# Kernel tuning notes

Measured on AMD Instinct MI355X. Metric: run time of the kernel, lower is better.

## Reference

```python
import jax, jax.numpy as jnp
import numpy as np

OUT_FEATURES = 512
IN_FEATURES = 512


def _unfold_tt(G1, G2):
    # G1: (1, do0, r, di0), G2: (r, do1, 1, di1)
    # einsum 'abcd,cefg->abefdg' then reshape -> (out_features, in_features)
    W = jnp.einsum('abcd,cefg->abefdg', G1, G2)
    return W.reshape(OUT_FEATURES, IN_FEATURES)


def setup_inputs() -> dict:
    key = jax.random.key(0)
    ks = jax.random.split(key, 5)
    std = np.sqrt(2.0 / IN_FEATURES).astype(np.float32)
    x = jax.random.normal(ks[0], (8, 4096, 2 * IN_FEATURES), dtype=jnp.float32)
    G1_R = jax.random.uniform(ks[1], (1, 32, 4, 32), jnp.float32, -std, std)
    G2_R = jax.random.uniform(ks[2], (4, 16, 1, 16), jnp.float32, -std, std)
    G1_I = jax.random.uniform(ks[3], (1, 32, 4, 32), jnp.float32, -std, std)
    G2_I = jax.random.uniform(ks[4], (4, 16, 1, 16), jnp.float32, -std, std)
    bias_real = jnp.zeros((OUT_FEATURES,), jnp.float32)
    bias_imag = jnp.zeros((OUT_FEATURES,), jnp.float32)
    return {"x": x, "G1_R": G1_R, "G2_R": G2_R, "G1_I": G1_I, "G2_I": G2_I,
            "bias_real": bias_real, "bias_imag": bias_imag}


def reference(x, G1_R, G2_R, G1_I, G2_I, bias_real, bias_imag):
    W_real = _unfold_tt(G1_R, G2_R)  # (out, in)
    W_imag = _unfold_tt(G1_I, G2_I)
    x_real, x_imag = jnp.split(x, 2, axis=-1)
    # F.linear(x, W, b) = x @ W.T + b
    out_real = x_real @ W_real.T - x_imag @ W_imag.T + bias_real
    out_imag = x_real @ W_imag.T + x_imag @ W_real.T + bias_imag
    return jnp.concatenate([out_real, out_imag], axis=-1)
```

## Files before the change

kernel.cpp:

```cpp
#include <hip/hip_runtime.h>
#include <hip/hip_bf16.h>
#include <stdint.h>


typedef _Float16 half8 __attribute__((ext_vector_type(8)));
typedef _Float16 half4v __attribute__((ext_vector_type(4)));
typedef float f32x4 __attribute__((ext_vector_type(4)));

typedef __attribute__((address_space(3))) void* lds_ptr_t;
typedef const __attribute__((address_space(1))) void* gbl_ptr_t;

__device__ __forceinline__ void gload_lds16(const void* g, void* s) {
  __builtin_amdgcn_global_load_lds((gbl_ptr_t)g, (lds_ptr_t)s, 16, 0, 0);
}

__global__ void build_bt(const float* __restrict__ G1R, const float* __restrict__ G2R,
                         const float* __restrict__ G1I, const float* __restrict__ G2I,
                         _Float16* __restrict__ BT) {
  int idx = blockIdx.x * 256 + threadIdx.x;
  int n = idx >> 10, k = idx & 1023;
  int o = n & 511, i = k & 511;
  bool imagOut = n >= 512, kHi = k >= 512;
  const float* G1;
  const float* G2;
  float sign = 1.0f;
  if (imagOut == kHi) { G1 = G1R; G2 = G2R; }
  else { G1 = G1I; G2 = G2I; if (!imagOut) sign = -1.0f; }
  int b = o >> 4, e = o & 15, d = i >> 4, g = i & 15;
  float w = 0.0f;
#pragma unroll
  for (int c = 0; c < 4; ++c)
    w += G1[b * 128 + c * 32 + d] * G2[c * 256 + e * 16 + g];
  BT[idx] = (_Float16)(sign * w);
}

__global__ __launch_bounds__(256, 2) void tt_gemm(
    const float* __restrict__ A,
    const _Float16* __restrict__ BT,
    const float* __restrict__ bias_r, const float* __restrict__ bias_i,
    float* __restrict__ C) {
  __shared__ __align__(16) _Float16 Als[128 * 32];
  __shared__ __align__(16) _Float16 Bls[128 * 32];

  const int tid = threadIdx.x;
  const int bid = blockIdx.x;
  const int bid2 = (bid & 7) * 256 + (bid >> 3);
  const int mt = bid2 >> 3, nt = bid2 & 7;
  const int row0 = mt * 128, col0 = nt * 128;

  const int lane = tid & 63, wid = tid >> 6;
  const int wm = wid >> 1, wn = wid & 1;
  const int lr = lane & 15, lq = lane >> 4;

  f32x4 acc[4][4] = {};

  const int brow_base = wid * 32 + (lane >> 2);
  const int bk = (lane & 3) * 8;

  const float* Abase = A + (size_t)row0 * 1024;

  for (int kt = 0; kt < 32; ++kt) {
    const int k0 = kt * 32;
    float4 va[4];
#pragma unroll
    for (int i = 0; i < 4; ++i) {
      int fid = i * 256 + tid;
      int ar = fid >> 3, aq = fid & 7;
      va[i] = *(const float4*)(Abase + (size_t)ar * 1024 + k0 + aq * 4);
    }
    __syncthreads();
#pragma unroll
    for (int i = 0; i < 4; ++i) {
      int fid = i * 256 + tid;
      int ar = fid >> 3, aq = fid & 7;
      half4v h = { (_Float16)va[i].x, (_Float16)va[i].y,
                   (_Float16)va[i].z, (_Float16)va[i].w };
      *(half4v*)&Als[ar * 32 + aq * 4] = h;
    }
#pragma unroll
    for (int j = 0; j < 2; ++j) {
      gload_lds16(BT + (size_t)(col0 + brow_base + j * 16) * 1024 + k0 + bk,
                  (char*)Bls + (wid * 2 + j) * 1024);
    }
    __syncthreads();
    half8 af[4], bf[4];
#pragma unroll
    for (int m = 0; m < 4; ++m)
      af[m] = *(const half8*)&Als[(wm * 64 + m * 16 + lr) * 32 + lq * 8];
#pragma unroll
    for (int n = 0; n < 4; ++n)
      bf[n] = *(const half8*)&Bls[(wn * 64 + n * 16 + lr) * 32 + lq * 8];
#pragma unroll
    for (int m = 0; m < 4; ++m)
#pragma unroll
      for (int n = 0; n < 4; ++n)
        acc[m][n] = __builtin_amdgcn_mfma_f32_16x16x32_f16(af[m], bf[n], acc[m][n], 0, 0, 0);
  }

#pragma unroll
  for (int n = 0; n < 4; ++n) {
    int col = col0 + wn * 64 + n * 16 + lr;
    float bias = (col < 512) ? bias_r[col] : bias_i[col - 512];
#pragma unroll
    for (int m = 0; m < 4; ++m) {
      int r0 = row0 + wm * 64 + m * 16 + lq * 4;
#pragma unroll
      for (int r = 0; r < 4; ++r)
        C[(size_t)(r0 + r) * 1024 + col] = acc[m][n][r] + bias;
    }
  }
}

extern "C" void kernel_launch(void* const* d_in, const int* in_sizes, int n_in,
                              void* d_out, int out_size, void* d_ws, size_t ws_size,
                              hipStream_t stream) {
  const float* x   = (const float*)d_in[0];
  const float* G1R = (const float*)d_in[1];
  const float* G2R = (const float*)d_in[2];
  const float* G1I = (const float*)d_in[3];
  const float* G2I = (const float*)d_in[4];
  const float* br  = (const float*)d_in[5];
  const float* bi  = (const float*)d_in[6];
  float* out = (float*)d_out;
  _Float16* BT = (_Float16*)d_ws;

  build_bt<<<4096, 256, 0, stream>>>(G1R, G2R, G1I, G2I, BT);
  tt_gemm<<<2048, 256, 0, stream>>>(x, BT, br, bi, out);
}
```

Before: 116.9 us.

## Enlarge GEMM tiles to 256x256, double-buffer LDS, pre-swizzle B image, interleave loads with MFMA

The fused complex weight matrix is now written as a tiled, XOR-swizzled LDS image, so each block can copy whole B tiles straight into shared memory without bank conflicts. The GEMM moves to 256x256 tiles with 512 threads, a K step of 64 and double-buffered LDS. Global loads for A and B are split into phases and interleaved with MFMA sub-blocks under s_setprio and explicit barriers. The aim is to hide memory latency and cut sync overhead per FLOP, at the cost of much higher register and LDS use (128 KB LDS per block) and lower occupancy.

```diff
diff --git a/kernel.cpp b/kernel.cpp
--- a/kernel.cpp
+++ b/kernel.cpp
@@ -14,16 +14,23 @@
   __builtin_amdgcn_global_load_lds((gbl_ptr_t)g, (lds_ptr_t)s, 16, 0, 0);
 }
 
+#define BAR() __builtin_amdgcn_s_barrier()
+#define PRIO1() __builtin_amdgcn_s_setprio(1)
+#define PRIO0() __builtin_amdgcn_s_setprio(0)
+
 __global__ void build_bt(const float* __restrict__ G1R, const float* __restrict__ G2R,
                          const float* __restrict__ G1I, const float* __restrict__ G2I,
-                         _Float16* __restrict__ BT) {
+                         _Float16* __restrict__ BTimg) {
   int idx = blockIdx.x * 256 + threadIdx.x;
-  int n = idx >> 10, k = idx & 1023;
+  int kcol = idx & 63;
+  int row  = (idx >> 6) & 255;
+  int kt   = (idx >> 14) & 15;
+  int nt   = idx >> 18;
+  int n = nt * 256 + row;
+  int k = kt * 64 + kcol;
   int o = n & 511, i = k & 511;
   bool imagOut = n >= 512, kHi = k >= 512;
-  const float* G1;
-  const float* G2;
-  float sign = 1.0f;
+  const float* G1; const float* G2; float sign = 1.0f;
   if (imagOut == kHi) { G1 = G1R; G2 = G2R; }
   else { G1 = G1I; G2 = G2I; if (!imagOut) sign = -1.0f; }
   int b = o >> 4, e = o & 15, d = i >> 4, g = i & 15;
@@ -31,82 +38,133 @@
 #pragma unroll
   for (int c = 0; c < 4; ++c)
     w += G1[b * 128 + c * 32 + d] * G2[c * 256 + e * 16 + g];
-  BT[idx] = (_Float16)(sign * w);
+  size_t byteoff = ((size_t)(nt * 16 + kt) << 15) + (size_t)row * 128
+                 + ((kcol * 2) ^ ((row & 7) << 4));
+  *(_Float16*)((char*)BTimg + byteoff) = (_Float16)(sign * w);
 }
 
-__global__ __launch_bounds__(256, 2) void tt_gemm(
+__global__ __launch_bounds__(512, 2) void tt_gemm(
     const float* __restrict__ A,
-    const _Float16* __restrict__ BT,
+    const _Float16* __restrict__ Bimg,
     const float* __restrict__ bias_r, const float* __restrict__ bias_i,
     float* __restrict__ C) {
-  __shared__ __align__(16) _Float16 Als[128 * 32];
-  __shared__ __align__(16) _Float16 Bls[128 * 32];
+  __shared__ __align__(16) _Float16 Als[2][16384];
+  __shared__ __align__(16) _Float16 Bls[2][16384];
 
   const int tid = threadIdx.x;
   const int bid = blockIdx.x;
-  const int bid2 = (bid & 7) * 256 + (bid >> 3);
-  const int mt = bid2 >> 3, nt = bid2 & 7;
-  const int row0 = mt * 128, col0 = nt * 128;
+  const int bid2 = (bid & 7) * 64 + (bid >> 3);
+  const int mt = bid2 >> 2, nt = bid2 & 3;
+  const int row0 = mt * 256, col0 = nt * 256;
 
   const int lane = tid & 63, wid = tid >> 6;
-  const int wm = wid >> 1, wn = wid & 1;
+  const int wm = wid >> 2, wn = wid & 3;
   const int lr = lane & 15, lq = lane >> 4;
 
-  f32x4 acc[4][4] = {};
-
-  const int brow_base = wid * 32 + (lane >> 2);
-  const int bk = (lane & 3) * 8;
-
+  const int arow = tid >> 4;
+  const int acol = (tid & 15) * 4;
   const float* Abase = A + (size_t)row0 * 1024;
 
-  for (int kt = 0; kt < 32; ++kt) {
-    const int k0 = kt * 32;
-    float4 va[4];
+  f32x4 acc[8][4] = {};
+  float4 areg[8];
+  half8 afr[4][2], bfr0[2][2], bfr1[2][2];
+
+  auto aissue = [&](int t, int i0) {
 #pragma unroll
     for (int i = 0; i < 4; ++i) {
-      int fid = i * 256 + tid;
-      int ar = fid >> 3, aq = fid & 7;
-      va[i] = *(const float4*)(Abase + (size_t)ar * 1024 + k0 + aq * 4);
+      int ii = i0 + i;
+      areg[ii] = *(const float4*)(Abase + (size_t)(ii * 32 + arow) * 1024 + t * 64 + acol);
     }
-    __syncthreads();
+  };
+  auto awrite = [&](int cb, int i0) {
 #pragma unroll
     for (int i = 0; i < 4; ++i) {
-      int fid = i * 256 + tid;
-      int ar = fid >> 3, aq = fid & 7;
-      half4v h = { (_Float16)va[i].x, (_Float16)va[i].y,
-                   (_Float16)va[i].z, (_Float16)va[i].w };
-      *(half4v*)&Als[ar * 32 + aq * 4] = h;
+      int ii = i0 + i;
+      int row = ii * 32 + arow;
+      int byte = row * 128 + (((tid & 15) * 8) ^ ((row & 7) << 4));
+      half4v h = { (_Float16)areg[ii].x, (_Float16)areg[ii].y,
+                   (_Float16)areg[ii].z, (_Float16)areg[ii].w };
+      *(half4v*)((char*)&Als[cb][0] + byte) = h;
     }
+  };
+  auto bissue = [&](int t, int cb) {
+    const char* src = (const char*)Bimg + (((size_t)nt * 16 + t) << 15) + wid * 4096 + lane * 16;
+    char* dst = (char*)&Bls[cb][0] + wid * 4096;
 #pragma unroll
-    for (int j = 0; j < 2; ++j) {
-      gload_lds16(BT + (size_t)(col0 + brow_base + j * 16) * 1024 + k0 + bk,
-                  (char*)Bls + (wid * 2 + j) * 1024);
-    }
-    __syncthreads();
-    half8 af[4], bf[4];
+    for (int j = 0; j < 4; ++j)
+      gload_lds16(src + j * 1024, dst + j * 1024);
+  };
+  auto lda = [&](int cb, int mh) {
 #pragma unroll
-    for (int m = 0; m < 4; ++m)
-      af[m] = *(const half8*)&Als[(wm * 64 + m * 16 + lr) * 32 + lq * 8];
+    for (int mf = 0; mf < 4; ++mf)
 #pragma unroll
-    for (int n = 0; n < 4; ++n)
-      bf[n] = *(const half8*)&Bls[(wn * 64 + n * 16 + lr) * 32 + lq * 8];
+      for (int kk = 0; kk < 2; ++kk) {
+        int row = wm * 128 + mh * 64 + mf * 16 + lr;
+        int byte = row * 128 + ((kk * 64 + lq * 16) ^ ((row & 7) << 4));
+        afr[mf][kk] = *(const half8*)((const char*)&Als[cb][0] + byte);
+      }
+  };
+  auto ldb = [&](int cb, int nh, half8 (&bf)[2][2]) {
 #pragma unroll
-    for (int m = 0; m < 4; ++m)
+    for (int j = 0; j < 2; ++j)
 #pragma unroll
-      for (int n = 0; n < 4; ++n)
-        acc[m][n] = __builtin_amdgcn_mfma_f32_16x16x32_f16(af[m], bf[n], acc[m][n], 0, 0, 0);
+      for (int kk = 0; kk < 2; ++kk) {
+        int row = wn * 64 + (nh * 2 + j) * 16 + lr;
+        int byte = row * 128 + ((kk * 64 + lq * 16) ^ ((row & 7) << 4));
+        bf[j][kk] = *(const half8*)((const char*)&Bls[cb][0] + byte);
+      }
+  };
+  auto mma = [&](int mh, int nh, half8 (&bf)[2][2]) {
+#pragma unroll
+    for (int mf = 0; mf < 4; ++mf)
+#pragma unroll
+      for (int j = 0; j < 2; ++j)
+#pragma unroll
+        for (int kk = 0; kk < 2; ++kk)
+          acc[mh * 4 + mf][nh * 2 + j] = __builtin_amdgcn_mfma_f32_16x16x32_f16(
+              afr[mf][kk], bf[j][kk], acc[mh * 4 + mf][nh * 2 + j], 0, 0, 0);
+  };
+
+  aissue(0, 0); aissue(0, 4);
+  bissue(0, 0);
+  awrite(0, 0); awrite(0, 4);
+  asm volatile("s_waitcnt vmcnt(0) lgkmcnt(0)" ::: "memory");
+  BAR();
+
+  for (int t = 0; t < 16; ++t) {
+    const int c = t & 1, c2 = c ^ 1;
+    const bool pf = (t < 15);
+    lda(c, 0); ldb(c, 0, bfr0);
+    if (pf) aissue(t + 1, 0);
+    BAR();
+    PRIO1(); mma(0, 0, bfr0); PRIO0();
+    BAR();
+    ldb(c, 1, bfr1);
+    if (pf) aissue(t + 1, 4);
+    BAR();
+    PRIO1(); mma(0, 1, bfr1); PRIO0();
+    BAR();
+    lda(c, 1);
+    if (pf) { bissue(t + 1, c2); awrite(c2, 0); }
+    BAR();
+    PRIO1(); mma(1, 1, bfr1); PRIO0();
+    BAR();
+    if (pf) awrite(c2, 4);
+    PRIO1(); mma(1, 0, bfr0); PRIO0();
+    asm volatile("s_waitcnt vmcnt(0) lgkmcnt(0)" ::: "memory");
+    BAR();
   }
 
 #pragma unroll
-  for (int n = 0; n < 4; ++n) {
-    int col = col0 + wn * 64 + n * 16 + lr;
+  for (int fn = 0; fn < 4; ++fn) {
+    int col = col0 + wn * 64 + fn * 16 + lr;
     float bias = (col < 512) ? bias_r[col] : bias_i[col - 512];
 #pragma unroll
-    for (int m = 0; m < 4; ++m) {
-      int r0 = row0 + wm * 64 + m * 16 + lq * 4;
+    for (int fm = 0; fm < 8; ++fm) {
+      int r0 = row0 + wm * 128 + fm * 16 + lq * 4;
 #pragma unroll
       for (int r = 0; r < 4; ++r)
-        C[(size_t)(r0 + r) * 1024 + col] = acc[m][n][r] + bias;
+        C[(size_t)(r0 + r) * 1024 + col] = acc[fm][fn][r] + bias;
     }
   }
 }
@@ -122,8 +180,8 @@
   const float* br  = (const float*)d_in[5];
   const float* bi  = (const float*)d_in[6];
   float* out = (float*)d_out;
-  _Float16* BT = (_Float16*)d_ws;
+  _Float16* BTimg = (_Float16*)d_ws;
 
-  build_bt<<<4096, 256, 0, stream>>>(G1R, G2R, G1I, G2I, BT);
-  tt_gemm<<<2048, 256, 0, stream>>>(x, BT, br, bi, out);
+  build_bt<<<4096, 256, 0, stream>>>(G1R, G2R, G1I, G2I, BTimg);
+  tt_gemm<<<512, 512, 0, stream>>>(x, BTimg, br, bi, out);
 }
```

Result: slower. 136.9 us (+17.1%).

## Pre-tile fp16 A/B images and use double-buffered 256x256 GEMM pipeline

Applied to the files above, without the earlier changes.

Adds a pre-pass that converts x to fp16 and writes it, along with the unfolded weight, into swizzled 64-wide K tiles, so the GEMM can stage both operands straight into LDS with global_load_lds. The GEMM moves to 256x256 tiles with 512 threads, double-buffered LDS, interleaved MFMA quarters, barriers and s_setprio to overlap loads with compute. The extra conversion pass writes and rereads a 64 MB intermediate, and if the workspace is too small the old path is used instead.

```diff
diff --git a/kernel.cpp b/kernel.cpp
--- a/kernel.cpp
+++ b/kernel.cpp
@@ -14,16 +14,161 @@
   __builtin_amdgcn_global_load_lds((gbl_ptr_t)g, (lds_ptr_t)s, 16, 0, 0);
 }
 
+#define BARF() asm volatile("s_barrier" ::: "memory")
+#define VMCNT0() asm volatile("s_waitcnt vmcnt(0)" ::: "memory")
+#define PRIO1() __builtin_amdgcn_s_setprio(1)
+#define PRIO0() __builtin_amdgcn_s_setprio(0)
+
+
 __global__ void build_bt(const float* __restrict__ G1R, const float* __restrict__ G2R,
                          const float* __restrict__ G1I, const float* __restrict__ G2I,
-                         _Float16* __restrict__ BT) {
+                         _Float16* __restrict__ BTimg) {
+  int idx = blockIdx.x * 256 + threadIdx.x;
+  int kcol = idx & 63;
+  int row  = (idx >> 6) & 255;
+  int kt   = (idx >> 14) & 15;
+  int nt   = idx >> 18;
+  int n = nt * 256 + row;
+  int k = kt * 64 + kcol;
+  int o = n & 511, i = k & 511;
+  bool imagOut = n >= 512, kHi = k >= 512;
+  const float* G1; const float* G2; float sign = 1.0f;
+  if (imagOut == kHi) { G1 = G1R; G2 = G2R; }
+  else { G1 = G1I; G2 = G2I; if (!imagOut) sign = -1.0f; }
+  int b = o >> 4, e = o & 15, d = i >> 4, g = i & 15;
+  float w = 0.0f;
+#pragma unroll
+  for (int c = 0; c < 4; ++c)
+    w += G1[b * 128 + c * 32 + d] * G2[c * 256 + e * 16 + g];
+  size_t byteoff = ((size_t)(nt * 16 + kt) << 15) + (size_t)row * 128
+                 + ((kcol * 2) ^ ((row & 7) << 4));
+  *(_Float16*)((char*)BTimg + byteoff) = (_Float16)(sign * w);
+}
+
+__global__ __launch_bounds__(256) void build_at(const float* __restrict__ A,
+                                                _Float16* __restrict__ Aimg) {
+  const int tid = threadIdx.x;
+  const int kt = blockIdx.x & 15, mt = blockIdx.x >> 4;
+  const float* src = A + (size_t)mt * 256 * 1024 + kt * 64;
+  char* dst = (char*)Aimg + ((size_t)(mt * 16 + kt) << 15);
+  const int cg = tid & 15;
+  const int rb = tid >> 4;
+#pragma unroll
+  for (int r = 0; r < 16; ++r) {
+    int row = rb + r * 16;
+    float4 v = *(const float4*)(src + (size_t)row * 1024 + cg * 4);
+    half4v h = { (_Float16)v.x, (_Float16)v.y, (_Float16)v.z, (_Float16)v.w };
+    *(half4v*)(dst + row * 128 + ((cg * 8) ^ ((row & 7) << 4))) = h;
+  }
+}
+
+__global__ __launch_bounds__(512, 2) void tt_gemm(
+    const _Float16* __restrict__ Aimg, const _Float16* __restrict__ Bimg,
+    const float* __restrict__ bias_r, const float* __restrict__ bias_i,
+    float* __restrict__ C) {
+  __shared__ __align__(16) _Float16 Als[2][16384];
+  __shared__ __align__(16) _Float16 Bls[2][16384];
+
+  const int tid = threadIdx.x;
+  const int bid = blockIdx.x;
+  const int bid2 = (bid & 7) * 64 + (bid >> 3);
+  const int mt = bid2 >> 2, nt = bid2 & 3;
+
+  const int lane = tid & 63, wid = tid >> 6;
+  const int wm = wid >> 2, wn = wid & 3;
+  const int lr = lane & 15, lq = lane >> 4;
+
+  f32x4 acc[8][4] = {};
+  half8 afr0[4][2], afr1[4][2], bfr0[2][2], bfr1[2][2];
+
+  const char* Abase = (const char*)Aimg + ((size_t)mt << 19);
+  const char* Bbase = (const char*)Bimg + ((size_t)nt << 19);
+  const int soff = wid * 1024 + lane * 16;
+  const int doff = wid * 1024;
+
+  auto stage = [&](const char* base, int t, _Float16* ldsbuf) {
+    const char* s = base + ((size_t)t << 15) + soff;
+    char* d = (char*)ldsbuf + doff;
+#pragma unroll
+    for (int j = 0; j < 4; ++j)
+      gload_lds16(s + j * 8192, d + j * 8192);
+  };
+  auto lda = [&](const _Float16* buf, int mh, half8 (&af)[4][2]) {
+#pragma unroll
+    for (int mf = 0; mf < 4; ++mf)
+#pragma unroll
+      for (int kk = 0; kk < 2; ++kk) {
+        int row = wm * 128 + mh * 64 + mf * 16 + lr;
+        int byte = row * 128 + ((kk * 64 + lq * 16) ^ ((row & 7) << 4));
+        af[mf][kk] = *(const half8*)((const char*)buf + byte);
+      }
+  };
+  auto ldb = [&](const _Float16* buf, int nh, half8 (&bf)[2][2]) {
+#pragma unroll
+    for (int j = 0; j < 2; ++j)
+#pragma unroll
+      for (int kk = 0; kk < 2; ++kk) {
+        int row = wn * 64 + (nh * 2 + j) * 16 + lr;
+        int byte = row * 128 + ((kk * 64 + lq * 16) ^ ((row & 7) << 4));
+        bf[j][kk] = *(const half8*)((const char*)buf + byte);
+      }
+  };
+  auto mmaq = [&](half8 (&af)[4][2], half8 (&bf)[2][2], int mb, int nb) {
+#pragma unroll
+    for (int mf = 0; mf < 4; ++mf)
+#pragma unroll
+      for (int j = 0; j < 2; ++j)
+#pragma unroll
+        for (int kk = 0; kk < 2; ++kk)
+          acc[mb + mf][nb + j] = __builtin_amdgcn_mfma_f32_16x16x32_f16(
+              af[mf][kk], bf[j][kk], acc[mb + mf][nb + j], 0, 0, 0);
+  };
+
+  stage(Abase, 0, Als[0]);
+  stage(Bbase, 0, Bls[0]);
+  VMCNT0();
+  BARF();
+
+  for (int t = 0; t < 16; ++t) {
+    const int c = t & 1;
+    _Float16* Ac = Als[c];  _Float16* Bc = Bls[c];
+    _Float16* An = Als[c ^ 1]; _Float16* Bn = Bls[c ^ 1];
+    const bool pf = (t < 15);
+    lda(Ac, 0, afr0); ldb(Bc, 0, bfr0);
+    if (pf) stage(Abase, t + 1, An);
+    BARF(); PRIO1(); mmaq(afr0, bfr0, 0, 0); PRIO0(); BARF();
+    ldb(Bc, 1, bfr1);
+    if (pf) stage(Bbase, t + 1, Bn);
+    BARF(); PRIO1(); mmaq(afr0, bfr1, 0, 2); PRIO0(); BARF();
+    lda(Ac, 1, afr1);
+    BARF(); PRIO1(); mmaq(afr1, bfr1, 4, 2); PRIO0(); BARF();
+    VMCNT0();
+    BARF(); PRIO1(); mmaq(afr1, bfr0, 4, 0); PRIO0(); BARF();
+  }
+
+  const int row0 = mt * 256, col0 = nt * 256;
+#pragma unroll
+  for (int fn = 0; fn < 4; ++fn) {
+    int col = col0 + wn * 64 + fn * 16 + lr;
+    float bias = (col < 512) ? bias_r[col] : bias_i[col - 512];
+#pragma unroll
+    for (int fm = 0; fm < 8; ++fm) {
+      int r0 = row0 + wm * 128 + (fm >> 2) * 64 + (fm & 3) * 16 + lq * 4;
+#pragma unroll
+      for (int r = 0; r < 4; ++r)
+        C[(size_t)(r0 + r) * 1024 + col] = acc[fm][fn][r] + bias;
+    }
+  }
+}
+
+__global__ void build_bt_flat(const float* __restrict__ G1R, const float* __restrict__ G2R,
+                              const float* __restrict__ G1I, const float* __restrict__ G2I,
+                              _Float16* __restrict__ BT) {
   int idx = blockIdx.x * 256 + threadIdx.x;
   int n = idx >> 10, k = idx & 1023;
   int o = n & 511, i = k & 511;
   bool imagOut = n >= 512, kHi = k >= 512;
-  const float* G1;
-  const float* G2;
-  float sign = 1.0f;
+  const float* G1; const float* G2; float sign = 1.0f;
   if (imagOut == kHi) { G1 = G1R; G2 = G2R; }
   else { G1 = G1I; G2 = G2I; if (!imagOut) sign = -1.0f; }
   int b = o >> 4, e = o & 15, d = i >> 4, g = i & 15;
@@ -34,31 +179,24 @@
   BT[idx] = (_Float16)(sign * w);
 }
 
-__global__ __launch_bounds__(256, 2) void tt_gemm(
-    const float* __restrict__ A,
-    const _Float16* __restrict__ BT,
+__global__ __launch_bounds__(256, 2) void tt_gemm_fb(
+    const float* __restrict__ A, const _Float16* __restrict__ BT,
     const float* __restrict__ bias_r, const float* __restrict__ bias_i,
     float* __restrict__ C) {
   __shared__ __align__(16) _Float16 Als[128 * 32];
   __shared__ __align__(16) _Float16 Bls[128 * 32];
-
   const int tid = threadIdx.x;
   const int bid = blockIdx.x;
   const int bid2 = (bid & 7) * 256 + (bid >> 3);
   const int mt = bid2 >> 3, nt = bid2 & 7;
   const int row0 = mt * 128, col0 = nt * 128;
-
   const int lane = tid & 63, wid = tid >> 6;
   const int wm = wid >> 1, wn = wid & 1;
   const int lr = lane & 15, lq = lane >> 4;
-
   f32x4 acc[4][4] = {};
-
   const int brow_base = wid * 32 + (lane >> 2);
   const int bk = (lane & 3) * 8;
-
   const float* Abase = A + (size_t)row0 * 1024;
-
   for (int kt = 0; kt < 32; ++kt) {
     const int k0 = kt * 32;
     float4 va[4];
@@ -78,10 +216,9 @@
       *(half4v*)&Als[ar * 32 + aq * 4] = h;
     }
 #pragma unroll
-    for (int j = 0; j < 2; ++j) {
+    for (int j = 0; j < 2; ++j)
       gload_lds16(BT + (size_t)(col0 + brow_base + j * 16) * 1024 + k0 + bk,
                   (char*)Bls + (wid * 2 + j) * 1024);
-    }
     __syncthreads();
     half8 af[4], bf[4];
 #pragma unroll
@@ -96,7 +233,6 @@
       for (int n = 0; n < 4; ++n)
         acc[m][n] = __builtin_amdgcn_mfma_f32_16x16x32_f16(af[m], bf[n], acc[m][n], 0, 0, 0);
   }
-
 #pragma unroll
   for (int n = 0; n < 4; ++n) {
     int col = col0 + wn * 64 + n * 16 + lr;
@@ -122,8 +258,18 @@
   const float* br  = (const float*)d_in[5];
   const float* bi  = (const float*)d_in[6];
   float* out = (float*)d_out;
-  _Float16* BT = (_Float16*)d_ws;
-
-  build_bt<<<4096, 256, 0, stream>>>(G1R, G2R, G1I, G2I, BT);
-  tt_gemm<<<2048, 256, 0, stream>>>(x, BT, br, bi, out);
-}
+
+  const size_t BIMG_BYTES = 2u << 20;
+  const size_t AIMG_BYTES = (size_t)64 << 20;
+  if (ws_size >= BIMG_BYTES + AIMG_BYTES) {
+    _Float16* Bimg = (_Float16*)d_ws;
+    _Float16* Aimg = (_Float16*)((char*)d_ws + BIMG_BYTES);
+    build_bt<<<4096, 256, 0, stream>>>(G1R, G2R, G1I, G2I, Bimg);
+    build_at<<<2048, 256, 0, stream>>>(x, Aimg);
+    tt_gemm<<<512, 512, 0, stream>>>(Aimg, Bimg, br, bi, out);
+  } else {
+    _Float16* BT = (_Float16*)d_ws;
+    build_bt_flat<<<4096, 256, 0, stream>>>(G1R, G2R, G1I, G2I, BT);
+    tt_gemm_fb<<<2048, 256, 0, stream>>>(x, BT, br, bi, out);
+  }
+}
```

Result: slower. 130.6 us (+11.7%).

## Double-buffer LDS tiles with register prefetch and pre-tiled B layout

Applied to the files above, without the earlier changes.

Splits A and B LDS staging into two buffers so the next k-tile's A conversion-write and B direct-to-LDS load overlap the current tile's MFMA work, with manual waitcnt and barrier control replacing two syncthreads per iteration. A is prefetched two tiles ahead into registers. build_bt now writes B in a tile-contiguous layout so each wave fetches contiguous 1KB chunks. Launch bounds allow three blocks per CU, at the cost of doubled LDS use and more register pressure from hand-written synchronisation.

```diff
diff --git a/kernel.cpp b/kernel.cpp
--- a/kernel.cpp
+++ b/kernel.cpp
@@ -4,7 +4,6 @@
 
 
 typedef _Float16 half8 __attribute__((ext_vector_type(8)));
-typedef _Float16 half4v __attribute__((ext_vector_type(4)));
 typedef float f32x4 __attribute__((ext_vector_type(4)));
 
 typedef __attribute__((address_space(3))) void* lds_ptr_t;
@@ -14,16 +13,25 @@
   __builtin_amdgcn_global_load_lds((gbl_ptr_t)g, (lds_ptr_t)s, 16, 0, 0);
 }
 
+#define BARF() asm volatile("s_barrier" ::: "memory")
+#define LGKM0() asm volatile("s_waitcnt lgkmcnt(0)" ::: "memory")
+#define VMC4() asm volatile("s_waitcnt vmcnt(4)" ::: "memory")
+#define VMC0() asm volatile("s_waitcnt vmcnt(0)" ::: "memory")
+#define FENCE() asm volatile("" ::: "memory")
+
 __global__ void build_bt(const float* __restrict__ G1R, const float* __restrict__ G2R,
                          const float* __restrict__ G1I, const float* __restrict__ G2I,
                          _Float16* __restrict__ BT) {
   int idx = blockIdx.x * 256 + threadIdx.x;
-  int n = idx >> 10, k = idx & 1023;
+  int col = idx & 31;
+  int row = (idx >> 5) & 127;
+  int kt  = (idx >> 12) & 31;
+  int nt  = idx >> 17;
+  int n = nt * 128 + row;
+  int k = kt * 32 + col;
   int o = n & 511, i = k & 511;
   bool imagOut = n >= 512, kHi = k >= 512;
-  const float* G1;
-  const float* G2;
-  float sign = 1.0f;
+  const float* G1; const float* G2; float sign = 1.0f;
   if (imagOut == kHi) { G1 = G1R; G2 = G2R; }
   else { G1 = G1I; G2 = G2I; if (!imagOut) sign = -1.0f; }
   int b = o >> 4, e = o & 15, d = i >> 4, g = i & 15;
@@ -34,13 +42,13 @@
   BT[idx] = (_Float16)(sign * w);
 }
 
-__global__ __launch_bounds__(256, 2) void tt_gemm(
+__global__ __launch_bounds__(256, 3) void tt_gemm(
     const float* __restrict__ A,
-    const _Float16* __restrict__ BT,
+    const _Float16* __restrict__ Bimg,
     const float* __restrict__ bias_r, const float* __restrict__ bias_i,
     float* __restrict__ C) {
-  __shared__ __align__(16) _Float16 Als[128 * 32];
-  __shared__ __align__(16) _Float16 Bls[128 * 32];
+  __shared__ __align__(16) _Float16 Als[2][4096];
+  __shared__ __align__(16) _Float16 Bls[2][4096];
 
   const int tid = threadIdx.x;
   const int bid = blockIdx.x;
@@ -53,60 +61,84 @@
   const int lr = lane & 15, lq = lane >> 4;
 
   f32x4 acc[4][4] = {};
-
-  const int brow_base = wid * 32 + (lane >> 2);
-  const int bk = (lane & 3) * 8;
+  float4 areg[4];
+  half8 afr[4], bfr[4];
 
   const float* Abase = A + (size_t)row0 * 1024;
+  const char* Bbase = (const char*)Bimg + ((size_t)nt << 18);
+  const int arow = tid >> 1;
+  const int ahalf = (tid & 1) * 16;
+
+  auto aload = [&](int kt) {
+#pragma unroll
+    for (int q = 0; q < 4; ++q)
+      areg[q] = *(const float4*)(Abase + (size_t)arow * 1024 + kt * 32 + ahalf + q * 4);
+  };
+  auto awrite = [&](_Float16* buf) {
+    half8 h0 = { (_Float16)areg[0].x, (_Float16)areg[0].y, (_Float16)areg[0].z, (_Float16)areg[0].w,
+                 (_Float16)areg[1].x, (_Float16)areg[1].y, (_Float16)areg[1].z, (_Float16)areg[1].w };
+    half8 h1 = { (_Float16)areg[2].x, (_Float16)areg[2].y, (_Float16)areg[2].z, (_Float16)areg[2].w,
+                 (_Float16)areg[3].x, (_Float16)areg[3].y, (_Float16)areg[3].z, (_Float16)areg[3].w };
+    char* d = (char*)buf + arow * 64 + ahalf * 2;
+    *(half8*)d = h0;
+    *(half8*)(d + 16) = h1;
+  };
+  auto bstage = [&](int kt, _Float16* buf) {
+    const char* s = Bbase + kt * 8192 + wid * 1024 + lane * 16;
+    char* d = (char*)buf + wid * 1024;
+    gload_lds16(s, d);
+    gload_lds16(s + 4096, d + 4096);
+  };
+  auto frd = [&](const _Float16* Ab, const _Float16* Bb) {
+#pragma unroll
+    for (int mf = 0; mf < 4; ++mf)
+      afr[mf] = *(const half8*)((const char*)Ab + (wm * 64 + mf * 16 + lr) * 64 + lq * 16);
+#pragma unroll
+    for (int nf = 0; nf < 4; ++nf)
+      bfr[nf] = *(const half8*)((const char*)Bb + (wn * 64 + nf * 16 + lr) * 64 + lq * 16);
+  };
+
+  aload(0);
+  FENCE();
+  awrite(Als[0]);
+  bstage(0, Bls[0]);
+  FENCE();
+  aload(1);
+  VMC4();
+  LGKM0();
+  BARF();
 
   for (int kt = 0; kt < 32; ++kt) {
-    const int k0 = kt * 32;
-    float4 va[4];
+    const int c = kt & 1, o = c ^ 1;
+    frd(Als[c], Bls[c]);
+    if (kt < 31) {
+      awrite(Als[o]);
+      bstage(kt + 1, Bls[o]);
+    }
+    FENCE();
+    if (kt < 30) aload(kt + 2);
+    FENCE();
 #pragma unroll
-    for (int i = 0; i < 4; ++i) {
-      int fid = i * 256 + tid;
-      int ar = fid >> 3, aq = fid & 7;
-      va[i] = *(const float4*)(Abase + (size_t)ar * 1024 + k0 + aq * 4);
-    }
-    __syncthreads();
+    for (int mf = 0; mf < 4; ++mf)
 #pragma unroll
-    for (int i = 0; i < 4; ++i) {
-      int fid = i * 256 + tid;
-      int ar = fid >> 3, aq = fid & 7;
-      half4v h = { (_Float16)va[i].x, (_Float16)va[i].y,
-                   (_Float16)va[i].z, (_Float16)va[i].w };
-      *(half4v*)&Als[ar * 32 + aq * 4] = h;
-    }
-#pragma unroll
-    for (int j = 0; j < 2; ++j) {
-      gload_lds16(BT + (size_t)(col0 + brow_base + j * 16) * 1024 + k0 + bk,
-                  (char*)Bls + (wid * 2 + j) * 1024);
-    }
-    __syncthreads();
-    half8 af[4], bf[4];
-#pragma unroll
-    for (int m = 0; m < 4; ++m)
-      af[m] = *(const half8*)&Als[(wm * 64 + m * 16 + lr) * 32 + lq * 8];
-#pragma unroll
-    for (int n = 0; n < 4; ++n)
-      bf[n] = *(const half8*)&Bls[(wn * 64 + n * 16 + lr) * 32 + lq * 8];
-#pragma unroll
-    for (int m = 0; m < 4; ++m)
-#pragma unroll
-      for (int n = 0; n < 4; ++n)
-        acc[m][n] = __builtin_amdgcn_mfma_f32_16x16x32_f16(af[m], bf[n], acc[m][n], 0, 0, 0);
+      for (int nf = 0; nf < 4; ++nf)
+        acc[mf][nf] = __builtin_amdgcn_mfma_f32_16x16x32_f16(
+            afr[mf], bfr[nf], acc[mf][nf], 0, 0, 0);
+    if (kt < 30) { VMC4(); }
+    else if (kt == 30) { VMC0(); }
+    if (kt < 31) { LGKM0(); BARF(); }
   }
 
 #pragma unroll
-  for (int n = 0; n < 4; ++n) {
-    int col = col0 + wn * 64 + n * 16 + lr;
+  for (int nf = 0; nf < 4; ++nf) {
+    int col = col0 + wn * 64 + nf * 16 + lr;
     float bias = (col < 512) ? bias_r[col] : bias_i[col - 512];
 #pragma unroll
-    for (int m = 0; m < 4; ++m) {
-      int r0 = row0 + wm * 64 + m * 16 + lq * 4;
+    for (int mf = 0; mf < 4; ++mf) {
+      int r0 = row0 + wm * 64 + mf * 16 + lq * 4;
 #pragma unroll
       for (int r = 0; r < 4; ++r)
-        C[(size_t)(r0 + r) * 1024 + col] = acc[m][n][r] + bias;
+        C[(size_t)(r0 + r) * 1024 + col] = acc[mf][nf][r] + bias;
     }
   }
 }
```

After: 125.0 us. 1.07x slower.
